# Kernel optimization log

Measured on AMD Instinct MI355X. Metric: run time of the kernel, lower is better.

The kernel has to match this reference:

```python
import jax, jax.numpy as jnp
import numpy as np

B, S, DIM = 2, 2048, 2048
H, KVH, HD = 16, 4, 128
G = H // KVH  # GQA groups = 4
THETA = 10000.0


def setup_inputs() -> dict:
    key = jax.random.key(0)
    k0, k1, k2, k3, k4 = jax.random.split(key, 5)
    x = jax.random.normal(k0, (B, S, DIM), jnp.float32)
    # RoPE table: [max_seq_len, head_dim//2, 2] holding (cos, sin)
    inv_freq = 1.0 / (THETA ** (jnp.arange(0, HD, 2, dtype=jnp.float32) / HD))
    angles = jnp.outer(jnp.arange(S, dtype=jnp.float32), inv_freq)  # [S, HD//2]
    freqs_cis = jnp.stack([jnp.cos(angles), jnp.sin(angles)], axis=-1)
    sc = 0.02
    wq = jax.random.normal(k1, (H * HD, DIM), jnp.float32) * sc
    wk = jax.random.normal(k2, (KVH * HD, DIM), jnp.float32) * sc
    wv = jax.random.normal(k3, (KVH * HD, DIM), jnp.float32) * sc
    wo = jax.random.normal(k4, (DIM, H * HD), jnp.float32) * sc
    return {"x": x, "freqs_cis": freqs_cis, "wq": wq, "wk": wk, "wv": wv, "wo": wo}


def apply_rope(x, freqs_cis):
    # x: [B, S, h, HD]; freqs_cis: [max_S, HD//2, 2]
    s = x.shape[1]
    xr = x.astype(jnp.float32).reshape(*x.shape[:-1], -1, 2)  # [B,S,h,HD//2,2]
    cos = freqs_cis[:s, :, 0][None, :, None, :]  # [1,S,1,HD//2]
    sin = freqs_cis[:s, :, 1][None, :, None, :]
    x0, x1 = xr[..., 0], xr[..., 1]
    out = jnp.stack([x0 * cos - x1 * sin, x0 * sin + x1 * cos], axis=-1)
    return out.reshape(x.shape).astype(x.dtype)


def reference(x, freqs_cis, wq, wk, wv, wo):
    b, s, d = x.shape
    q = (x @ wq.T).reshape(b, s, H, HD)
    k = (x @ wk.T).reshape(b, s, KVH, HD)
    v = (x @ wv.T).reshape(b, s, KVH, HD)
    q = apply_rope(q, freqs_cis)
    k = apply_rope(k, freqs_cis)
    # GQA expand: repeat_interleave along head dim
    k = jnp.repeat(k, G, axis=2)  # [b,s,H,HD]
    v = jnp.repeat(v, G, axis=2)
    q = jnp.swapaxes(q, 1, 2)  # [b,H,s,HD]
    k = jnp.swapaxes(k, 1, 2)
    v = jnp.swapaxes(v, 1, 2)
    scale = 1.0 / jnp.sqrt(jnp.asarray(HD, dtype=q.dtype))
    scores = jnp.einsum('bhqd,bhkd->bhqk', q, k) * scale  # [b,H,s,s]
    causal = jnp.tril(jnp.ones((s, s), dtype=bool))
    scores = jnp.where(causal[None, None], scores, jnp.finfo(scores.dtype).min)
    probs = jax.nn.softmax(scores, axis=-1)
    attn = jnp.einsum('bhqk,bhkd->bhqd', probs, v)  # [b,H,s,HD]
    attn = jnp.swapaxes(attn, 1, 2).reshape(b, s, H * HD)
    return attn @ wo.T
```

## Files before the change

kernel.cpp:

```cpp
#include <hip/hip_runtime.h>
#include <stdint.h>

#define B_ 2
#define S_ 2048
#define DIM_ 2048
#define H_ 16
#define KVH_ 4
#define HD_ 128

typedef short short8 __attribute__((ext_vector_type(8)));
typedef float f4 __attribute__((ext_vector_type(4)));
typedef unsigned short u16;

#define KSCALE (0.08838834764831845f * 1.4426950408889634f)

__device__ __forceinline__ float bf2f(u16 u) {
    union { unsigned int i; float f; } c; c.i = ((unsigned int)u) << 16; return c.f;
}
__device__ __forceinline__ u16 f2bf(float f) {
    union { float f; unsigned int i; } c; c.f = f;
    return (u16)((c.i + 0x7fffu + ((c.i >> 16) & 1u)) >> 16);
}

#define GLDS16(gp, lp) \
    __builtin_amdgcn_global_load_lds((const __attribute__((address_space(1))) unsigned int*)(gp), \
                                     (__attribute__((address_space(3))) unsigned int*)(lp), 16, 0, 0)

__global__ void cast4_kernel(const float* __restrict__ in, u16* __restrict__ out, int n4) {
    int i = blockIdx.x * blockDim.x + threadIdx.x;
    if (i < n4) {
        float4 v = ((const float4*)in)[i];
        ushort4 o;
        o.x = f2bf(v.x); o.y = f2bf(v.y); o.z = f2bf(v.z); o.w = f2bf(v.w);
        ((ushort4*)out)[i] = o;
    }
}

template<bool OUT_BF16>
__global__ __launch_bounds__(256) void gemm_bt(const u16* __restrict__ A,
                                               const u16* __restrict__ W,
                                               void* __restrict__ Cout,
                                               int M, int N, int K) {
    __shared__ u16 As[128 * 32];
    __shared__ u16 Bs[128 * 32];
    int t = threadIdx.x, lane = t & 63, w = t >> 6;
    int quad = lane >> 4, l16 = lane & 15;
    int wm = w & 1, wn = w >> 1;
    size_t m0 = (size_t)blockIdx.y * 128, n0 = (size_t)blockIdx.x * 128;

    int c0 = w * 2;
    int ar = c0 * 16 + (lane >> 2);
    int ac = (lane & 3) * 8;
    const u16* Abase = A + (m0 + ar) * (size_t)K + ac;
    const u16* Bbase = W + (n0 + ar) * (size_t)K + ac;
    u16* Adst = As + c0 * 512;
    u16* Bdst = Bs + c0 * 512;

    f4 acc[4][4];
    #pragma unroll
    for (int i = 0; i < 4; i++)
        #pragma unroll
        for (int j = 0; j < 4; j++) acc[i][j] = (f4){0.f, 0.f, 0.f, 0.f};

    int nk = K >> 5;
    for (int kt = 0; kt < nk; kt++) {
        const u16* ga = Abase + kt * 32;
        const u16* gb = Bbase + kt * 32;
        GLDS16(ga, Adst);
        GLDS16(ga + 16 * (size_t)K, Adst + 512);
        GLDS16(gb, Bdst);
        GLDS16(gb + 16 * (size_t)K, Bdst + 512);
        __syncthreads();
        short8 a[4], b[4];
        #pragma unroll
        for (int i = 0; i < 4; i++) a[i] = *(const short8*)&As[(wm * 64 + i * 16 + l16) * 32 + quad * 8];
        #pragma unroll
        for (int j = 0; j < 4; j++) b[j] = *(const short8*)&Bs[(wn * 64 + j * 16 + l16) * 32 + quad * 8];
        #pragma unroll
        for (int i = 0; i < 4; i++)
            #pragma unroll
            for (int j = 0; j < 4; j++)
                acc[i][j] = __builtin_amdgcn_mfma_f32_16x16x32_bf16(a[i], b[j], acc[i][j], 0, 0, 0);
        __syncthreads();
    }
    #pragma unroll
    for (int i = 0; i < 4; i++) {
        size_t row = m0 + wm * 64 + i * 16 + quad * 4;
        #pragma unroll
        for (int j = 0; j < 4; j++) {
            size_t col = n0 + wn * 64 + j * 16 + l16;
            #pragma unroll
            for (int r = 0; r < 4; r++) {
                if (OUT_BF16) ((u16*)Cout)[(row + r) * N + col] = f2bf(acc[i][j][r]);
                else          ((float*)Cout)[(row + r) * N + col] = acc[i][j][r];
            }
        }
    }
}

__global__ void rope_q(u16* __restrict__ QKV, const float* __restrict__ freqs) {
    int pc = blockIdx.x * 256 + threadIdx.x;
    int row = blockIdx.y;
    int s = row & (S_ - 1);
    int hd2 = pc & 63;
    float2 cs = ((const float2*)freqs)[s * 64 + hd2];
    ushort2* pp = (ushort2*)(QKV + (size_t)row * 3072);
    ushort2 v = pp[pc];
    float x0 = bf2f(v.x), x1 = bf2f(v.y);
    ushort2 ov;
    ov.x = f2bf((x0 * cs.x - x1 * cs.y) * KSCALE);
    ov.y = f2bf((x0 * cs.y + x1 * cs.x) * KSCALE);
    pp[pc] = ov;
}

__global__ __launch_bounds__(256) void pack_k(const u16* __restrict__ QKV,
                                              const float* __restrict__ freqs,
                                              u16* __restrict__ Kp) {
    int gid = blockIdx.x * 256 + threadIdx.x;
    int lane = gid & 63;
    int fid = (gid >> 6) & 15;
    int kt = (gid >> 10) & 31;
    int bk = gid >> 15;
    int b = bk >> 2, kvh = bk & 3;
    int n = fid >> 2, c = fid & 3;
    int l16 = lane & 15, quad = lane >> 4;
    int s = kt * 64 + n * 16 + l16;
    const u16* src = QKV + (size_t)(b * 2048 + s) * 3072 + 2048 + kvh * 128 + c * 32 + quad * 8;
    short8 v = *(const short8*)src;
    short8 o;
    #pragma unroll
    for (int jp = 0; jp < 4; jp++) {
        int hd2 = c * 16 + quad * 4 + jp;
        float2 cw = ((const float2*)freqs)[s * 64 + hd2];
        float x0 = bf2f((u16)v[2 * jp]), x1 = bf2f((u16)v[2 * jp + 1]);
        o[2 * jp]     = (short)f2bf(x0 * cw.x - x1 * cw.y);
        o[2 * jp + 1] = (short)f2bf(x0 * cw.y + x1 * cw.x);
    }
    *(short8*)&Kp[(size_t)gid * 8] = o;
}

__global__ __launch_bounds__(256) void pack_v(const u16* __restrict__ QKV, u16* __restrict__ Vp) {
    __shared__ u16 L[64 * 136];
    int bid = blockIdx.x;
    int bk = bid & 7, kt = bid >> 3;
    int b = bk >> 2, kvh = bk & 3;
    int t = threadIdx.x;
    const u16* src = QKV + (size_t)(b * 2048 + kt * 64) * 3072 + 2560 + kvh * 128;
    #pragma unroll
    for (int it = 0; it < 4; it++) {
        int idx = t + it * 256;
        int r = idx >> 4, c = idx & 15;
        *(short8*)&L[r * 136 + c * 8] = *(const short8*)(src + (size_t)r * 3072 + c * 8);
    }
    __syncthreads();
    u16* dst = Vp + ((size_t)bk * 32 + kt) * 8192;
    #pragma unroll
    for (int it = 0; it < 4; it++) {
        int idx = t + it * 256;
        int fid = idx >> 6, lane = idx & 63;
        int nt = fid >> 1, kc = fid & 1;
        int l16 = lane & 15, quad = lane >> 4;
        int hd = nt * 16 + l16;
        int s0 = kc * 32 + quad * 8;
        short8 v;
        #pragma unroll
        for (int j = 0; j < 8; j++) v[j] = (short)L[(s0 + j) * 136 + hd];
        *(short8*)&dst[(size_t)idx * 8] = v;
    }
}

__global__ __launch_bounds__(256, 4) void attn_kernel(const u16* __restrict__ QKV,
                                                      const u16* __restrict__ Kp,
                                                      const u16* __restrict__ Vp,
                                                      u16* __restrict__ Ob) {
    __shared__ u16 Ks[16 * 512];
    __shared__ u16 Vs[16 * 512];
    __shared__ u16 Ps[4 * 1024];
    int bid = blockIdx.x;
    int bk = bid & 7;
    int qt = 127 - (bid >> 3);
    int b = bk >> 2, kvh = bk & 3;
    int t = threadIdx.x, lane = t & 63, w = t >> 6, quad = lane >> 4, l16 = lane & 15;
    int l7 = l16 & 7, hi = l16 >> 3;
    int h = kvh * 4 + w;

    short8 qf[4];
    {
        const u16* qp = QKV + ((size_t)(b * S_ + qt * 16 + l16)) * 3072 + h * HD_ + quad * 8;
        #pragma unroll
        for (int c = 0; c < 4; c++) qf[c] = *(const short8*)(qp + c * 32);
    }
    short8 ones;
    #pragma unroll
    for (int j = 0; j < 8; j++) ones[j] = (short)0x3F80;

    float m_i = -3e38f;
    f4 ls = (f4){0.f, 0.f, 0.f, 0.f};
    f4 o[8];
    #pragma unroll
    for (int n = 0; n < 8; n++) o[n] = (f4){0.f, 0.f, 0.f, 0.f};

    const u16* Kpb = Kp + (size_t)bk * 32 * 8192;
    const u16* Vpb = Vp + (size_t)bk * 32 * 8192;
    u16* P = Ps + w * 1024;
    int nkt = (qt >> 2) + 1;

    for (int kt = 0; kt < nkt; kt++) {
        {
            const u16* ks = Kpb + (size_t)kt * 8192 + (w * 4) * 512 + lane * 8;
            const u16* vs = Vpb + (size_t)kt * 8192 + (w * 4) * 512 + lane * 8;
            #pragma unroll
            for (int i = 0; i < 4; i++) {
                GLDS16(ks + i * 512, &Ks[(w * 4 + i) * 512]);
                GLDS16(vs + i * 512, &Vs[(w * 4 + i) * 512]);
            }
        }
        __syncthreads();

        f4 sc[4];
        #pragma unroll
        for (int n = 0; n < 4; n++) sc[n] = (f4){0.f, 0.f, 0.f, 0.f};
        #pragma unroll
        for (int n = 0; n < 4; n++) {
            #pragma unroll
            for (int c = 0; c < 4; c++) {
                short8 kf = *(const short8*)&Ks[(n * 4 + c) * 512 + lane * 8];
                sc[n] = __builtin_amdgcn_mfma_f32_16x16x32_bf16(qf[c], kf, sc[n], 0, 0, 0);
            }
        }
        if (kt == nkt - 1) {
            int qrow0 = qt * 16 + quad * 4;
            #pragma unroll
            for (int n = 0; n < 4; n++) {
                int colg = kt * 64 + n * 16 + l16;
                #pragma unroll
                for (int r = 0; r < 4; r++)
                    sc[n][r] = (colg <= qrow0 + r) ? sc[n][r] : -3e38f;
            }
        }
        float gm = fmaxf(fmaxf(sc[0][0], sc[0][1]), fmaxf(sc[0][2], sc[0][3]));
        #pragma unroll
        for (int n = 1; n < 4; n++)
            gm = fmaxf(gm, fmaxf(fmaxf(sc[n][0], sc[n][1]), fmaxf(sc[n][2], sc[n][3])));
        #pragma unroll
        for (int off = 1; off < 64; off <<= 1) gm = fmaxf(gm, __shfl_xor(gm, off, 64));
        float mnew = fmaxf(m_i, gm);
        if (mnew > m_i) {
            float al = exp2f(m_i - mnew);
            m_i = mnew;
            #pragma unroll
            for (int r = 0; r < 4; r++) ls[r] *= al;
            #pragma unroll
            for (int nt = 0; nt < 8; nt++)
                #pragma unroll
                for (int r = 0; r < 4; r++) o[nt][r] *= al;
        }
        #pragma unroll
        for (int n = 0; n < 4; n++) {
            #pragma unroll
            for (int r = 0; r < 4; r++) {
                float p = exp2f(sc[n][r] - m_i);
                union { float f; unsigned int u; } cv; cv.f = p;
                int row = quad * 4 + r;
                int sw = (n * 2 + hi) ^ (row & 7);
                P[row * 64 + sw * 8 + l7] = (u16)(cv.u >> 16);
            }
        }
        __asm__ volatile("s_waitcnt lgkmcnt(0)" ::: "memory");

        #pragma unroll
        for (int kc = 0; kc < 2; kc++) {
            short8 af = *(const short8*)&P[l16 * 64 + (((kc * 4 + quad) ^ l7) << 3)];
            ls = __builtin_amdgcn_mfma_f32_16x16x32_bf16(af, ones, ls, 0, 0, 0);
            #pragma unroll
            for (int nt = 0; nt < 8; nt++) {
                short8 vf = *(const short8*)&Vs[(nt * 2 + kc) * 512 + lane * 8];
                o[nt] = __builtin_amdgcn_mfma_f32_16x16x32_bf16(af, vf, o[nt], 0, 0, 0);
            }
        }
        __syncthreads();
    }
    float rl[4];
    #pragma unroll
    for (int r = 0; r < 4; r++) rl[r] = 1.0f / ls[r];
    #pragma unroll
    for (int nt = 0; nt < 8; nt++)
        #pragma unroll
        for (int r = 0; r < 4; r++) {
            size_t row = (size_t)b * S_ + qt * 16 + quad * 4 + r;
            Ob[row * 2048 + h * HD_ + nt * 16 + l16] = f2bf(o[nt][r] * rl[r]);
        }
}

extern "C" void kernel_launch(void* const* d_in, const int* in_sizes, int n_in,
                              void* d_out, int out_size, void* d_ws, size_t ws_size,
                              hipStream_t stream) {
    const float* x     = (const float*)d_in[0];
    const float* freqs = (const float*)d_in[1];
    const float* wq    = (const float*)d_in[2];
    const float* wk    = (const float*)d_in[3];
    const float* wv    = (const float*)d_in[4];
    const float* wo    = (const float*)d_in[5];
    float* out = (float*)d_out;

    char* p = (char*)d_ws;
    u16* xb    = (u16*)p; p += (size_t)4096 * 2048 * 2;
    u16* wqkvb = (u16*)p; p += (size_t)3072 * 2048 * 2;
    u16* wob   = (u16*)p; p += (size_t)2048 * 2048 * 2;
    u16* QKVb  = (u16*)p; p += (size_t)4096 * 3072 * 2;
    u16* Kpb   = (u16*)p; p += (size_t)8 * 32 * 8192 * 2;
    u16* Vpb   = (u16*)p; p += (size_t)8 * 32 * 8192 * 2;
    u16* attnb = xb;

    cast4_kernel<<<8192, 256, 0, stream>>>(x, xb, 2097152);
    cast4_kernel<<<4096, 256, 0, stream>>>(wq, wqkvb, 1048576);
    cast4_kernel<<<1024, 256, 0, stream>>>(wk, wqkvb + (size_t)2048 * 2048, 262144);
    cast4_kernel<<<1024, 256, 0, stream>>>(wv, wqkvb + (size_t)2560 * 2048, 262144);
    cast4_kernel<<<4096, 256, 0, stream>>>(wo, wob, 1048576);

    gemm_bt<true><<<dim3(24, 32), 256, 0, stream>>>(xb, wqkvb, QKVb, 4096, 3072, 2048);

    rope_q<<<dim3(4, 4096), 256, 0, stream>>>(QKVb, freqs);

    pack_k<<<1024, 256, 0, stream>>>(QKVb, freqs, Kpb);
    pack_v<<<256, 256, 0, stream>>>(QKVb, Vpb);

    attn_kernel<<<1024, 256, 0, stream>>>(QKVb, Kpb, Vpb, attnb);

    gemm_bt<false><<<dim3(16, 32), 256, 0, stream>>>(attnb, wob, out, 4096, 2048, 2048);
}
```

Baseline: 345.6 us.

## Pair causal query tiles per attention block and merge cast kernels

The attention kernel now runs 512 blocks. Each block handles two query tiles, a long one (127-pr) and a short one (pr), so every block gets the same amount of causal work and the tail imbalance goes away. Occupancy is pinned to 2 waves per EU where it was 4 blocks before. The five fp32-to-bf16 cast launches become one kernel with branchy index dispatch, which removes launch overhead. The risks are lower occupancy and less latency hiding in the attention kernel.

New measurement: 324.0 us. 1.07x faster.

```diff
diff --git a/kernel.cpp b/kernel.cpp
--- a/kernel.cpp
+++ b/kernel.cpp
@@ -26,14 +26,21 @@
     __builtin_amdgcn_global_load_lds((const __attribute__((address_space(1))) unsigned int*)(gp), \
                                      (__attribute__((address_space(3))) unsigned int*)(lp), 16, 0, 0)
 
-__global__ void cast4_kernel(const float* __restrict__ in, u16* __restrict__ out, int n4) {
-    int i = blockIdx.x * blockDim.x + threadIdx.x;
-    if (i < n4) {
-        float4 v = ((const float4*)in)[i];
-        ushort4 o;
-        o.x = f2bf(v.x); o.y = f2bf(v.y); o.z = f2bf(v.z); o.w = f2bf(v.w);
-        ((ushort4*)out)[i] = o;
-    }
+__global__ void cast_all(const float* __restrict__ x,  const float* __restrict__ wq,
+                         const float* __restrict__ wk, const float* __restrict__ wv,
+                         const float* __restrict__ wo,
+                         u16* __restrict__ xb, u16* __restrict__ wqkvb, u16* __restrict__ wob) {
+    int i = blockIdx.x * 256 + threadIdx.x;
+    const float4* src; ushort4* dst; int j;
+    if (i < 2097152)      { src = (const float4*)x;  dst = (ushort4*)xb;                 j = i; }
+    else if (i < 3145728) { src = (const float4*)wq; dst = (ushort4*)wqkvb;              j = i - 2097152; }
+    else if (i < 3407872) { src = (const float4*)wk; dst = (ushort4*)wqkvb + 1048576;    j = i - 3145728; }
+    else if (i < 3670016) { src = (const float4*)wv; dst = (ushort4*)wqkvb + 1310720;    j = i - 3407872; }
+    else                  { src = (const float4*)wo; dst = (ushort4*)wob;                j = i - 3670016; }
+    float4 v = src[j];
+    ushort4 o;
+    o.x = f2bf(v.x); o.y = f2bf(v.y); o.z = f2bf(v.z); o.w = f2bf(v.w);
+    dst[j] = o;
 }
 
 template<bool OUT_BF16>
@@ -169,127 +176,131 @@
     }
 }
 
-__global__ __launch_bounds__(256, 4) void attn_kernel(const u16* __restrict__ QKV,
-                                                      const u16* __restrict__ Kp,
-                                                      const u16* __restrict__ Vp,
-                                                      u16* __restrict__ Ob) {
+__global__ __launch_bounds__(256) __attribute__((amdgpu_waves_per_eu(2, 2)))
+void attn_kernel(const u16* __restrict__ QKV,
+                 const u16* __restrict__ Kp,
+                 const u16* __restrict__ Vp,
+                 u16* __restrict__ Ob) {
     __shared__ u16 Ks[16 * 512];
     __shared__ u16 Vs[16 * 512];
     __shared__ u16 Ps[4 * 1024];
     int bid = blockIdx.x;
-    int bk = bid & 7;
-    int qt = 127 - (bid >> 3);
+    int bk = bid & 7, pr = bid >> 3;
     int b = bk >> 2, kvh = bk & 3;
     int t = threadIdx.x, lane = t & 63, w = t >> 6, quad = lane >> 4, l16 = lane & 15;
     int l7 = l16 & 7, hi = l16 >> 3;
     int h = kvh * 4 + w;
 
-    short8 qf[4];
-    {
-        const u16* qp = QKV + ((size_t)(b * S_ + qt * 16 + l16)) * 3072 + h * HD_ + quad * 8;
-        #pragma unroll
-        for (int c = 0; c < 4; c++) qf[c] = *(const short8*)(qp + c * 32);
-    }
     short8 ones;
     #pragma unroll
     for (int j = 0; j < 8; j++) ones[j] = (short)0x3F80;
-
-    float m_i = -3e38f;
-    f4 ls = (f4){0.f, 0.f, 0.f, 0.f};
-    f4 o[8];
-    #pragma unroll
-    for (int n = 0; n < 8; n++) o[n] = (f4){0.f, 0.f, 0.f, 0.f};
 
     const u16* Kpb = Kp + (size_t)bk * 32 * 8192;
     const u16* Vpb = Vp + (size_t)bk * 32 * 8192;
     u16* P = Ps + w * 1024;
-    int nkt = (qt >> 2) + 1;
-
-    for (int kt = 0; kt < nkt; kt++) {
+
+    for (int ph = 0; ph < 2; ph++) {
+        int qt = ph ? pr : 127 - pr;
+        int nkt = (qt >> 2) + 1;
+
+        short8 qf[4];
         {
-            const u16* ks = Kpb + (size_t)kt * 8192 + (w * 4) * 512 + lane * 8;
-            const u16* vs = Vpb + (size_t)kt * 8192 + (w * 4) * 512 + lane * 8;
-            #pragma unroll
-            for (int i = 0; i < 4; i++) {
-                GLDS16(ks + i * 512, &Ks[(w * 4 + i) * 512]);
-                GLDS16(vs + i * 512, &Vs[(w * 4 + i) * 512]);
-            }
+            const u16* qp = QKV + ((size_t)(b * S_ + qt * 16 + l16)) * 3072 + h * HD_ + quad * 8;
+            #pragma unroll
+            for (int c = 0; c < 4; c++) qf[c] = *(const short8*)(qp + c * 32);
         }
-        __syncthreads();
-
-        f4 sc[4];
-        #pragma unroll
-        for (int n = 0; n < 4; n++) sc[n] = (f4){0.f, 0.f, 0.f, 0.f};
-        #pragma unroll
-        for (int n = 0; n < 4; n++) {
-            #pragma unroll
-            for (int c = 0; c < 4; c++) {
-                short8 kf = *(const short8*)&Ks[(n * 4 + c) * 512 + lane * 8];
-                sc[n] = __builtin_amdgcn_mfma_f32_16x16x32_bf16(qf[c], kf, sc[n], 0, 0, 0);
-            }
+        float m_i = -3e38f;
+        f4 ls = (f4){0.f, 0.f, 0.f, 0.f};
+        f4 o[8];
+        #pragma unroll
+        for (int n = 0; n < 8; n++) o[n] = (f4){0.f, 0.f, 0.f, 0.f};
+
+        for (int kt = 0; kt < nkt; kt++) {
+            {
+                const u16* ks = Kpb + (size_t)kt * 8192 + (w * 4) * 512 + lane * 8;
+                const u16* vs = Vpb + (size_t)kt * 8192 + (w * 4) * 512 + lane * 8;
+                #pragma unroll
+                for (int i = 0; i < 4; i++) {
+                    GLDS16(ks + i * 512, &Ks[(w * 4 + i) * 512]);
+                    GLDS16(vs + i * 512, &Vs[(w * 4 + i) * 512]);
+                }
+            }
+            __syncthreads();
+
+            f4 sc[4];
+            #pragma unroll
+            for (int n = 0; n < 4; n++) sc[n] = (f4){0.f, 0.f, 0.f, 0.f};
+            #pragma unroll
+            for (int n = 0; n < 4; n++) {
+                #pragma unroll
+                for (int c = 0; c < 4; c++) {
+                    short8 kf = *(const short8*)&Ks[(n * 4 + c) * 512 + lane * 8];
+                    sc[n] = __builtin_amdgcn_mfma_f32_16x16x32_bf16(qf[c], kf, sc[n], 0, 0, 0);
+                }
+            }
+            if (kt == nkt - 1) {
+                int qrow0 = qt * 16 + quad * 4;
+                #pragma unroll
+                for (int n = 0; n < 4; n++) {
+                    int colg = kt * 64 + n * 16 + l16;
+                    #pragma unroll
+                    for (int r = 0; r < 4; r++)
+                        sc[n][r] = (colg <= qrow0 + r) ? sc[n][r] : -3e38f;
+                }
+            }
+            float gm = fmaxf(fmaxf(sc[0][0], sc[0][1]), fmaxf(sc[0][2], sc[0][3]));
+            #pragma unroll
+            for (int n = 1; n < 4; n++)
+                gm = fmaxf(gm, fmaxf(fmaxf(sc[n][0], sc[n][1]), fmaxf(sc[n][2], sc[n][3])));
+            #pragma unroll
+            for (int off = 1; off < 64; off <<= 1) gm = fmaxf(gm, __shfl_xor(gm, off, 64));
+            float mnew = fmaxf(m_i, gm);
+            if (mnew > m_i) {
+                float al = exp2f(m_i - mnew);
+                m_i = mnew;
+                #pragma unroll
+                for (int r = 0; r < 4; r++) ls[r] *= al;
+                #pragma unroll
+                for (int nt = 0; nt < 8; nt++)
+                    #pragma unroll
+                    for (int r = 0; r < 4; r++) o[nt][r] *= al;
+            }
+            #pragma unroll
+            for (int n = 0; n < 4; n++) {
+                #pragma unroll
+                for (int r = 0; r < 4; r++) {
+                    float p = exp2f(sc[n][r] - m_i);
+                    union { float f; unsigned int u; } cv; cv.f = p;
+                    int row = quad * 4 + r;
+                    int sw = (n * 2 + hi) ^ (row & 7);
+                    P[row * 64 + sw * 8 + l7] = (u16)(cv.u >> 16);
+                }
+            }
+            __asm__ volatile("s_waitcnt lgkmcnt(0)" ::: "memory");
+
+            #pragma unroll
+            for (int kc = 0; kc < 2; kc++) {
+                short8 af = *(const short8*)&P[l16 * 64 + (((kc * 4 + quad) ^ l7) << 3)];
+                ls = __builtin_amdgcn_mfma_f32_16x16x32_bf16(af, ones, ls, 0, 0, 0);
+                #pragma unroll
+                for (int nt = 0; nt < 8; nt++) {
+                    short8 vf = *(const short8*)&Vs[(nt * 2 + kc) * 512 + lane * 8];
+                    o[nt] = __builtin_amdgcn_mfma_f32_16x16x32_bf16(af, vf, o[nt], 0, 0, 0);
+                }
+            }
+            __syncthreads();
         }
-        if (kt == nkt - 1) {
-            int qrow0 = qt * 16 + quad * 4;
-            #pragma unroll
-            for (int n = 0; n < 4; n++) {
-                int colg = kt * 64 + n * 16 + l16;
-                #pragma unroll
-                for (int r = 0; r < 4; r++)
-                    sc[n][r] = (colg <= qrow0 + r) ? sc[n][r] : -3e38f;
-            }
-        }
-        float gm = fmaxf(fmaxf(sc[0][0], sc[0][1]), fmaxf(sc[0][2], sc[0][3]));
-        #pragma unroll
-        for (int n = 1; n < 4; n++)
-            gm = fmaxf(gm, fmaxf(fmaxf(sc[n][0], sc[n][1]), fmaxf(sc[n][2], sc[n][3])));
-        #pragma unroll
-        for (int off = 1; off < 64; off <<= 1) gm = fmaxf(gm, __shfl_xor(gm, off, 64));
-        float mnew = fmaxf(m_i, gm);
-        if (mnew > m_i) {
-            float al = exp2f(m_i - mnew);
-            m_i = mnew;
-            #pragma unroll
-            for (int r = 0; r < 4; r++) ls[r] *= al;
-            #pragma unroll
-            for (int nt = 0; nt < 8; nt++)
-                #pragma unroll
-                for (int r = 0; r < 4; r++) o[nt][r] *= al;
-        }
-        #pragma unroll
-        for (int n = 0; n < 4; n++) {
+        float rl[4];
+        #pragma unroll
+        for (int r = 0; r < 4; r++) rl[r] = 1.0f / ls[r];
+        #pragma unroll
+        for (int nt = 0; nt < 8; nt++)
             #pragma unroll
             for (int r = 0; r < 4; r++) {
-                float p = exp2f(sc[n][r] - m_i);
-                union { float f; unsigned int u; } cv; cv.f = p;
-                int row = quad * 4 + r;
-                int sw = (n * 2 + hi) ^ (row & 7);
-                P[row * 64 + sw * 8 + l7] = (u16)(cv.u >> 16);
-            }
-        }
-        __asm__ volatile("s_waitcnt lgkmcnt(0)" ::: "memory");
-
-        #pragma unroll
-        for (int kc = 0; kc < 2; kc++) {
-            short8 af = *(const short8*)&P[l16 * 64 + (((kc * 4 + quad) ^ l7) << 3)];
-            ls = __builtin_amdgcn_mfma_f32_16x16x32_bf16(af, ones, ls, 0, 0, 0);
-            #pragma unroll
-            for (int nt = 0; nt < 8; nt++) {
-                short8 vf = *(const short8*)&Vs[(nt * 2 + kc) * 512 + lane * 8];
-                o[nt] = __builtin_amdgcn_mfma_f32_16x16x32_bf16(af, vf, o[nt], 0, 0, 0);
-            }
-        }
-        __syncthreads();
-    }
-    float rl[4];
-    #pragma unroll
-    for (int r = 0; r < 4; r++) rl[r] = 1.0f / ls[r];
-    #pragma unroll
-    for (int nt = 0; nt < 8; nt++)
-        #pragma unroll
-        for (int r = 0; r < 4; r++) {
-            size_t row = (size_t)b * S_ + qt * 16 + quad * 4 + r;
-            Ob[row * 2048 + h * HD_ + nt * 16 + l16] = f2bf(o[nt][r] * rl[r]);
-        }
+                size_t row = (size_t)b * S_ + qt * 16 + quad * 4 + r;
+                Ob[row * 2048 + h * HD_ + nt * 16 + l16] = f2bf(o[nt][r] * rl[r]);
+            }
+    }
 }
 
 extern "C" void kernel_launch(void* const* d_in, const int* in_sizes, int n_in,
@@ -312,11 +323,7 @@
     u16* Vpb   = (u16*)p; p += (size_t)8 * 32 * 8192 * 2;
     u16* attnb = xb;
 
-    cast4_kernel<<<8192, 256, 0, stream>>>(x, xb, 2097152);
-    cast4_kernel<<<4096, 256, 0, stream>>>(wq, wqkvb, 1048576);
-    cast4_kernel<<<1024, 256, 0, stream>>>(wk, wqkvb + (size_t)2048 * 2048, 262144);
-    cast4_kernel<<<1024, 256, 0, stream>>>(wv, wqkvb + (size_t)2560 * 2048, 262144);
-    cast4_kernel<<<4096, 256, 0, stream>>>(wo, wob, 1048576);
+    cast_all<<<18432, 256, 0, stream>>>(x, wq, wk, wv, wo, xb, wqkvb, wob);
 
     gemm_bt<true><<<dim3(24, 32), 256, 0, stream>>>(xb, wqkvb, QKVb, 4096, 3072, 2048);
 
@@ -325,7 +332,7 @@
     pack_k<<<1024, 256, 0, stream>>>(QKVb, freqs, Kpb);
     pack_v<<<256, 256, 0, stream>>>(QKVb, Vpb);
 
-    attn_kernel<<<1024, 256, 0, stream>>>(QKVb, Kpb, Vpb, attnb);
+    attn_kernel<<<512, 256, 0, stream>>>(QKVb, Kpb, Vpb, attnb);
 
     gemm_bt<false><<<dim3(16, 32), 256, 0, stream>>>(attnb, wob, out, 4096, 2048, 2048);
 }
```
